# Kernel tuning notes

Measured on AMD Instinct MI355X. Metric: run time of the kernel, lower is better.

The kernel has to match this reference:

```python
import jax, jax.numpy as jnp
import numpy as np

QS, B, C, H, M = 512, 8, 1024, 16, 1536
HC = C // H
KS = QS  # xk = xv = xq (self-attention)


def setup_inputs() -> dict:
    key = jax.random.key(0)
    ks = jax.random.split(key, 16)
    scale = 1.0 / np.sqrt(C)
    xq = jax.random.normal(ks[0], (QS, B, C), jnp.float32)
    memory_kv = jax.random.normal(ks[1], (M, B, H, 2 * HC), jnp.float32)
    memory_length = jax.random.randint(ks[2], (B,), 0, M)
    pad = jax.random.randint(ks[3], (B,), 0, KS)
    mask = jnp.zeros((QS, KS, B), dtype=bool)
    Wq = jax.random.normal(ks[4], (C, C), jnp.float32) * scale
    bq = jax.random.normal(ks[5], (C,), jnp.float32) * 0.02
    Wk = jax.random.normal(ks[6], (C, C), jnp.float32) * scale
    bk = jax.random.normal(ks[7], (C,), jnp.float32) * 0.02
    Wv = jax.random.normal(ks[8], (C, C), jnp.float32) * scale
    bv = jax.random.normal(ks[9], (C,), jnp.float32) * 0.02
    Wo = jax.random.normal(ks[10], (C, C), jnp.float32) * scale
    bo = jax.random.normal(ks[11], (C,), jnp.float32) * 0.02
    return dict(xq=xq, pad=pad, mask=mask, memory_length=memory_length,
                memory_kv=memory_kv, Wq=Wq, bq=bq, Wk=Wk, bk=bk,
                Wv=Wv, bv=bv, Wo=Wo, bo=bo)


def _memory_attention(xq, pad, mask, memory_length, memory_kv,
                      Wq, bq, Wk, bk, Wv, bv, Wo, bo):
    qs, b, c = xq.shape
    m = memory_kv.shape[0]
    T = m + KS  # combined kv length (static upper bound = max(memory_length)+pad)

    # qkv projections (torch Linear: x @ W.T + b), layout (seq, batch, h, hc)
    q = (xq @ Wq.T + bq).reshape(qs, b, H, HC)
    k = (xq @ Wk.T + bk).reshape(KS, b, H, HC)
    v = (xq @ Wv.T + bv).reshape(KS, b, H, HC)

    # cat_padded_seqs as a static-shape gather: slot t of batch i is
    #   memory[t]        if t <  memory_length[i]
    #   new[t - len_i]   if t - len_i < pad[i]
    #   padding (masked) otherwise
    t = jnp.arange(T)[:, None]                      # [T,1]
    L = memory_length[None, :]                      # [1,b]
    in_mem = t < L                                  # [T,b]
    off = t - L                                     # [T,b] offset into new seq
    in_new = (off >= 0) & (off < pad[None, :])      # [T,b]
    idx_new = jnp.clip(off, 0, KS - 1)              # [T,b]

    mem_k = memory_kv[..., :HC]
    mem_v = memory_kv[..., HC:]
    mem_idx = jnp.minimum(jnp.arange(T), m - 1)     # [T]
    k_mem = mem_k[mem_idx]                          # [T,b,H,HC]
    v_mem = mem_v[mem_idx]

    gidx = jnp.broadcast_to(idx_new[:, :, None, None], (T, b, H, HC))
    k_new = jnp.take_along_axis(k, gidx, axis=0)    # [T,b,H,HC]
    v_new = jnp.take_along_axis(v, gidx, axis=0)

    sel = in_mem[:, :, None, None]
    k_comb = jnp.where(sel, k_mem, k_new)
    v_comb = jnp.where(sel, v_mem, v_new)

    # combined padding/user mask, True = masked out
    midx = jnp.broadcast_to(idx_new[None, :, :], (qs, T, b))
    user_m = jnp.take_along_axis(mask, midx, axis=1)        # [qs,T,b]
    comb_mask = jnp.where(in_mem[None], False,
                          jnp.where(in_new[None], user_m, True))

    # attention
    temperature = 1.0 / np.sqrt(HC)
    a = jnp.einsum('sbhc,tbhc->stbh', q, k_comb) * temperature
    a = jnp.where(comb_mask[:, :, :, None], -jnp.inf, a)
    p = jax.nn.softmax(a, axis=1)
    p = jnp.nan_to_num(p)  # fully-masked rows -> 0 (matches torch)
    x = jnp.einsum('stbh,tbhc->sbhc', p, v_comb).reshape(qs, b, c)
    return x @ Wo.T + bo


def reference(xq, pad, mask, memory_length, memory_kv,
              Wq, bq, Wk, bk, Wv, bv, Wo, bo):
    return _memory_attention(xq, pad, mask, memory_length, memory_kv,
                             Wq, bq, Wk, bk, Wv, bv, Wo, bo)
```

## Files before the change

### kernel.cpp

```cpp
#include <hip/hip_runtime.h>

#define QS_ 512
#define B_  8
#define C_  1024
#define H_  16
#define HC_ 64
#define M_  1536
#define KS_ 512
#define TMX 2048

typedef __attribute__((ext_vector_type(8))) short bf16x8;
typedef __attribute__((ext_vector_type(4))) float f32x4;

__device__ __forceinline__ short f2bf(float f) {
    unsigned u = __float_as_uint(f);
    unsigned r = (u + 0x7FFF + ((u >> 16) & 1)) >> 16;
    return (short)r;
}

__device__ __forceinline__ void gload_lds16(const void* g, void* l) {
    __builtin_amdgcn_global_load_lds(
        (const __attribute__((address_space(1))) unsigned int*)g,
        (__attribute__((address_space(3))) unsigned int*)l, 16, 0, 0);
}

__global__ __launch_bounds__(256) void prep_all(
    const float* __restrict__ xq,
    const float* __restrict__ w0, const float* __restrict__ w1,
    const float* __restrict__ w2, const float* __restrict__ w3,
    short* __restrict__ xqb,
    short* __restrict__ d0, short* __restrict__ d1,
    short* __restrict__ d2, short* __restrict__ d3,
    const float* __restrict__ mkv, short* __restrict__ kall,
    short* __restrict__ vall,
    const unsigned char* __restrict__ maskb, const int* __restrict__ mlen,
    const int* __restrict__ padv, unsigned char* __restrict__ mbits)
{
    __shared__ short T[64][72];
    const int bx = blockIdx.x;
    const int tid = threadIdx.x;

    if (bx < 4096) {
        int idx = bx * 256 + tid;
        const float* src; short* dst; int i;
        if (idx < 524288) { src = xq; dst = xqb; i = idx; }
        else {
            int sel = (idx >> 17) & 3;
            i = idx & 131071;
            src = sel == 0 ? w0 : sel == 1 ? w1 : sel == 2 ? w2 : w3;
            dst = sel == 0 ? d0 : sel == 1 ? d1 : sel == 2 ? d2 : d3;
        }
        const float4* s = (const float4*)src + (size_t)i * 2;
        float4 a = s[0], bq = s[1];
        short o[8];
        o[0] = f2bf(a.x);  o[1] = f2bf(a.y);  o[2] = f2bf(a.z);  o[3] = f2bf(a.w);
        o[4] = f2bf(bq.x); o[5] = f2bf(bq.y); o[6] = f2bf(bq.z); o[7] = f2bf(bq.w);
        *(uint4*)(dst + (size_t)i * 8) = *(uint4*)o;
        return;
    }

    if (bx < 7168) {
        const int idx = bx - 4096;
        const int tc = idx % 24;
        const int h  = (idx / 24) & 15;
        const int b  = idx / 384;
        const int L = mlen[b];
        const int tendb = L + padv[b];
        if (tc * 64 >= tendb) return;
        const int row = tid >> 2, part = tid & 3;
        const int t = tc * 64 + row;
        const int g = b * H_ + h;
        const bool skiprow = (t >= L) && (t < L + 512);
        short o[32];
        if (!skiprow) {
            const float4* src = (const float4*)(mkv + (((size_t)t * B_ + b) * H_ + h) * 128 + part * 32);
#pragma unroll
            for (int j = 0; j < 8; ++j) {
                float4 f = src[j];
                o[j * 4 + 0] = f2bf(f.x); o[j * 4 + 1] = f2bf(f.y);
                o[j * 4 + 2] = f2bf(f.z); o[j * 4 + 3] = f2bf(f.w);
            }
        } else {
#pragma unroll
            for (int j = 0; j < 32; ++j) o[j] = 0;
        }
        if (part < 2) {
            if (!skiprow) {
                short* d = kall + ((size_t)g * TMX + t) * 64 + part * 32;
#pragma unroll
                for (int j = 0; j < 4; ++j) ((uint4*)d)[j] = ((uint4*)o)[j];
            }
        } else {
            int hc0 = (part - 2) * 32;
#pragma unroll
            for (int j = 0; j < 32; ++j) T[hc0 + j][row] = o[j];
        }
        __syncthreads();
        const int hc = tid >> 2, seg = tid & 3;
        uint4 a = *(const uint4*)&T[hc][seg * 16];
        uint4 c = *(const uint4*)&T[hc][seg * 16 + 8];
        short* d = vall + ((size_t)g * HC_ + hc) * TMX + tc * 64 + seg * 16;
        ((uint4*)d)[0] = a; ((uint4*)d)[1] = c;
        return;
    }

    if (bx < 7296) {
        const int i = bx - 7168;
        const int b = i >> 4, h = i & 15;
        const int L = mlen[b], P = padv[b];
        const int te = L + P;
        const int z0 = max(1536, L + 512);
        const int z1 = min(2048, (te + 63) & ~63);
        if (z1 > z0) {
            const int g = b * 16 + h;
            const int hc = tid >> 2;
            short* rowp = vall + ((size_t)g * HC_ + hc) * TMX;
            for (int c = z0 + (tid & 3); c < z1; c += 4) rowp[c] = 0;
        }
        return;
    }

    {
        const int j = bx - 7296;
        const int b = j >> 6;
        const int q = (j & 63) * 8 + (tid >> 5);
        const int wordIdx = tid & 31;
        const int L = mlen[b], P = padv[b];
        const int tb = wordIdx * 64;
        unsigned long long w;
        if (tb + 63 < L) {
            w = 0ull;
        } else if (tb >= L + P) {
            w = ~0ull;
        } else {
            w = 0ull;
            const unsigned char* mq = maskb + (size_t)q * (KS_ * B_) + b;
#pragma unroll 4
            for (int k = 0; k < 64; ++k) {
                int t = tb + k;
                int bit;
                if (t < L) bit = 0;
                else {
                    int off = t - L;
                    bit = (off >= P) ? 1 : (mq[(size_t)off * B_] ? 1 : 0);
                }
                w |= (unsigned long long)bit << k;
            }
        }
        ((unsigned long long*)mbits)[(((size_t)(b * 512 + q)) << 5) + wordIdx] = w;
    }
}

template <int EPI>
__device__ __forceinline__ void gemm128_body(
    short (*As)[64], short (*Ws)[64],
    const short* __restrict__ A, const short* __restrict__ W,
    const float* __restrict__ bias, void* __restrict__ outv,
    int n0, int j0, float oscale, const int* __restrict__ mlen)
{
    const int tid  = threadIdx.x;
    const int lane = tid & 63;
    const int wave = tid >> 6;
    const int wm = (wave & 1) * 64;
    const int wn = (wave >> 1) * 64;
    const int lr = lane & 15;
    const int quad = lane >> 4;

    f32x4 acc[4][4];
#pragma unroll
    for (int i = 0; i < 4; ++i)
#pragma unroll
        for (int j = 0; j < 4; ++j)
            acc[i][j] = (f32x4){0.f, 0.f, 0.f, 0.f};

    for (int k0 = 0; k0 < C_; k0 += 64) {
#pragma unroll
        for (int p = 0; p < 4; ++p) {
            int flat = p * 256 + tid;
            int r = flat >> 3, c8 = (flat & 7) * 8;
            gload_lds16(A + (size_t)(n0 + r) * C_ + k0 + c8, (short*)As + flat * 8);
        }
#pragma unroll
        for (int p = 0; p < 4; ++p) {
            int flat = p * 256 + tid;
            int r = flat >> 3, c8 = (flat & 7) * 8;
            gload_lds16(W + (size_t)(j0 + r) * C_ + k0 + c8, (short*)Ws + flat * 8);
        }
        __syncthreads();
#pragma unroll
        for (int ks = 0; ks < 2; ++ks) {
            const int kk = ks * 32 + quad * 8;
            bf16x8 afrag[4], bfrag[4];
#pragma unroll
            for (int im = 0; im < 4; ++im)
                afrag[im] = *(const bf16x8*)&As[wm + im * 16 + lr][kk];
#pragma unroll
            for (int jn = 0; jn < 4; ++jn)
                bfrag[jn] = *(const bf16x8*)&Ws[wn + jn * 16 + lr][kk];
#pragma unroll
            for (int im = 0; im < 4; ++im)
#pragma unroll
                for (int jn = 0; jn < 4; ++jn)
                    acc[im][jn] = __builtin_amdgcn_mfma_f32_16x16x32_bf16(
                        afrag[im], bfrag[jn], acc[im][jn], 0, 0, 0);
        }
        __syncthreads();
    }

    if constexpr (EPI == 2 || EPI == 3) {
        int ml[8];
#pragma unroll
        for (int i = 0; i < 8; ++i) ml[i] = mlen[i];
#pragma unroll
        for (int jn = 0; jn < 4; ++jn) {
            const int col = j0 + wn + jn * 16 + lr;
            const int h = col >> 6, hc = col & 63;
            const float bv = bias[col];
#pragma unroll
            for (int im = 0; im < 4; ++im) {
                const int row = n0 + wm + im * 16 + quad * 4;
#pragma unroll
                for (int r = 0; r < 4; ++r) {
                    const int rr = row + r;
                    const int s = rr >> 3, b = rr & 7;
                    float v = acc[im][jn][r] + bv;
                    if (EPI == 2)
                        ((short*)outv)[((size_t)((b * 16 + h) * TMX) + ml[b] + s) * 64 + hc] = f2bf(v);
                    else
                        ((short*)outv)[((size_t)((b * 16 + h) * 64 + hc)) * TMX + ml[b] + s] = f2bf(v);
                }
            }
        }
    } else {
#pragma unroll
        for (int jn = 0; jn < 4; ++jn) {
            const int col = j0 + wn + jn * 16 + lr;
            const float bv = bias[col];
#pragma unroll
            for (int im = 0; im < 4; ++im) {
                const int row = n0 + wm + im * 16 + quad * 4;
#pragma unroll
                for (int r = 0; r < 4; ++r) {
                    float v = (acc[im][jn][r] + bv) * oscale;
                    if (EPI == 1)
                        ((short*)outv)[(size_t)(row + r) * C_ + col] = f2bf(v);
                    else
                        ((float*)outv)[(size_t)(row + r) * C_ + col] = v;
                }
            }
        }
    }
}

__global__ __launch_bounds__(256) void gemm128_f32(
    const short* __restrict__ A, const short* __restrict__ W,
    const float* __restrict__ bias, float* __restrict__ outv)
{
    __shared__ short As[128][64];
    __shared__ short Ws[128][64];
    gemm128_body<0>(As, Ws, A, W, bias, outv,
                    blockIdx.x * 128, blockIdx.y * 128, 1.0f, nullptr);
}

__global__ __launch_bounds__(256) void gemm128_qkv(
    const short* __restrict__ A,
    const short* __restrict__ Wq, const short* __restrict__ Wk,
    const short* __restrict__ Wv,
    const float* __restrict__ bq, const float* __restrict__ bk,
    const float* __restrict__ bv,
    short* __restrict__ oq, short* __restrict__ kall, short* __restrict__ vall,
    const int* __restrict__ mlen)
{
    __shared__ short As[128][64];
    __shared__ short Ws[128][64];
    const int sel = blockIdx.y >> 3;
    const int n0 = blockIdx.x * 128;
    const int j0 = (blockIdx.y & 7) * 128;
    if (sel == 0)
        gemm128_body<1>(As, Ws, A, Wq, bq, oq, n0, j0, 0.125f, nullptr);
    else if (sel == 1)
        gemm128_body<2>(As, Ws, A, Wk, bk, kall, n0, j0, 1.0f, mlen);
    else
        gemm128_body<3>(As, Ws, A, Wv, bv, vall, n0, j0, 1.0f, mlen);
}

__global__ __launch_bounds__(256, 4) void attn_block(
    const short* __restrict__ qb, const short* __restrict__ kall,
    const short* __restrict__ vall, const unsigned char* __restrict__ mbits,
    const int* __restrict__ mlen, const int* __restrict__ padv,
    short* __restrict__ xout)
{
    __shared__ short Ks[2][64][64];
    __shared__ short Vs[2][64][64];

    const int tid  = threadIdx.x;
    const int lane = tid & 63;
    const int wave = tid >> 6;
    const int lr   = lane & 15;
    const int quad = lane >> 4;
    const int bx = blockIdx.x;
    const int g  = ((bx >> 6) << 3) | (bx & 7);
    const int qg = (bx >> 3) & 7;
    const int b  = g >> 4, h = g & 15;
    const int tend = mlen[b] + padv[b];
    const float NEG = -1e30f;

    const int q = qg * 64 + wave * 16 + lr;

    const short* qrow = qb + ((size_t)q * B_ + b) * C_ + h * HC_;
    bf16x8 q0 = *(const bf16x8*)(qrow + quad * 8);
    bf16x8 q1 = *(const bf16x8*)(qrow + 32 + quad * 8);

    const char* kg = (const char*)(kall + (size_t)g * TMX * 64);
    const char* vg = (const char*)(vall + (size_t)g * HC_ * TMX);
    const unsigned char* mrow = mbits + ((size_t)(b * 512 + q) << 8);

    f32x4 O[4];
#pragma unroll
    for (int i = 0; i < 4; ++i) O[i] = (f32x4){0.f, 0.f, 0.f, 0.f};
    float mr = NEG, lsum = 0.f;

    const int nch = (tend + 63) >> 6;

    auto stage = [&](int t0, int buf) {
        char* KsB = (char*)Ks[buf];
        char* VsB = (char*)Vs[buf];
#pragma unroll
        for (int i = 0; i < 4; ++i) {
            int p = wave * 4 + i;
            int f = ((p & 7) << 6) + lane;
            int row = f >> 3;
            int c = ((f & 7) << 4) ^ ((row & 7) << 4);
            if (p < 8)
                gload_lds16(kg + (size_t)(t0 + row) * 128 + c,
                            KsB + (size_t)f * 16);
            else
                gload_lds16(vg + (size_t)row * (TMX * 2) + (size_t)t0 * 2 + c,
                            VsB + (size_t)f * 16);
        }
    };

    if (nch > 0) stage(0, 0);
    __syncthreads();

    int cur = 0;
    for (int ci = 0; ci < nch; ++ci) {
        const int t0 = ci << 6;

        unsigned long long mw = *(const unsigned long long*)(mrow + (t0 >> 3));

        if (ci + 1 < nch) stage((ci + 1) << 6, cur ^ 1);

        const char* KsB = (const char*)Ks[cur];
        const char* VsB = (const char*)Vs[cur];

        bf16x8 kf[4][2];
#pragma unroll
        for (int tt = 0; tt < 4; ++tt) {
            int t = tt * 16 + lr;
            int sw = (t & 7) << 4;
            kf[tt][0] = *(const bf16x8*)(KsB + t * 128 + ((quad * 16) ^ sw));
            kf[tt][1] = *(const bf16x8*)(KsB + t * 128 + ((64 + quad * 16) ^ sw));
        }

        __builtin_amdgcn_s_setprio(1);
        f32x4 S[4];
#pragma unroll
        for (int tt = 0; tt < 4; ++tt) {
            f32x4 z = (f32x4){0.f, 0.f, 0.f, 0.f};
            z = __builtin_amdgcn_mfma_f32_16x16x32_bf16(kf[tt][0], q0, z, 0, 0, 0);
            S[tt] = __builtin_amdgcn_mfma_f32_16x16x32_bf16(kf[tt][1], q1, z, 0, 0, 0);
        }
        __builtin_amdgcn_s_setprio(0);

        bf16x8 vf[4][2];
#pragma unroll
        for (int ht = 0; ht < 4; ++ht) {
            int hc = ht * 16 + lr;
            int sw = (hc & 7) << 4;
            vf[ht][0] = *(const bf16x8*)(VsB + hc * 128 + ((quad * 16) ^ sw));
            vf[ht][1] = *(const bf16x8*)(VsB + hc * 128 + ((64 + quad * 16) ^ sw));
        }

        float p4[4][4];
#pragma unroll
        for (int tt = 0; tt < 4; ++tt) {
            unsigned m4 = ((unsigned)(mw >> (tt * 16 + quad * 4))) & 15u;
#pragma unroll
            for (int r = 0; r < 4; ++r)
                p4[tt][r] = (m4 & (1u << r)) ? NEG : S[tt][r];
        }

        float rm = NEG;
#pragma unroll
        for (int tt = 0; tt < 4; ++tt)
#pragma unroll
            for (int r = 0; r < 4; ++r) rm = fmaxf(rm, p4[tt][r]);
        rm = fmaxf(rm, __shfl_xor(rm, 16, 64));
        rm = fmaxf(rm, __shfl_xor(rm, 32, 64));
        const float nm = fmaxf(fmaxf(mr, rm), -1e20f);
        const float al = __expf(mr - nm);
        float rs = 0.f;
#pragma unroll
        for (int tt = 0; tt < 4; ++tt)
#pragma unroll
            for (int r = 0; r < 4; ++r) {
                float e = __expf(p4[tt][r] - nm);
                p4[tt][r] = e;
                rs += e;
            }
        rs += __shfl_xor(rs, 16, 64);
        rs += __shfl_xor(rs, 32, 64);
        lsum = lsum * al + rs;
        mr = nm;
#pragma unroll
        for (int ht = 0; ht < 4; ++ht)
#pragma unroll
            for (int r = 0; r < 4; ++r) O[ht][r] *= al;

        bf16x8 pf[2];
        const int slA = ((quad & 1) * 2) * 16 + lr;
        const int slB = slA + 16;
        const unsigned sel = (quad & 2) ? 0x07060302u : 0x05040100u;
#pragma unroll
        for (int hf = 0; hf < 2; ++hf) {
            const int tt0 = hf * 2;
            unsigned pk[4];
#pragma unroll
            for (int r = 0; r < 4; ++r) {
                unsigned o;
                asm("v_cvt_pk_bf16_f32 %0, %1, %2"
                    : "=v"(o) : "v"(p4[tt0][r]), "v"(p4[tt0 + 1][r]));
                pk[r] = o;
            }
            unsigned uA[4], uB[4];
#pragma unroll
            for (int r = 0; r < 4; ++r) {
                uA[r] = (unsigned)__shfl((int)pk[r], slA, 64);
                uB[r] = (unsigned)__shfl((int)pk[r], slB, 64);
            }
            unsigned wv[4];
            wv[0] = __builtin_amdgcn_perm(uA[1], uA[0], sel);
            wv[1] = __builtin_amdgcn_perm(uA[3], uA[2], sel);
            wv[2] = __builtin_amdgcn_perm(uB[1], uB[0], sel);
            wv[3] = __builtin_amdgcn_perm(uB[3], uB[2], sel);
            pf[hf] = *(const bf16x8*)wv;
        }

        __builtin_amdgcn_s_setprio(1);
#pragma unroll
        for (int ht = 0; ht < 4; ++ht) {
            O[ht] = __builtin_amdgcn_mfma_f32_16x16x32_bf16(vf[ht][0], pf[0], O[ht], 0, 0, 0);
            O[ht] = __builtin_amdgcn_mfma_f32_16x16x32_bf16(vf[ht][1], pf[1], O[ht], 0, 0, 0);
        }
        __builtin_amdgcn_s_setprio(0);

        __syncthreads();
        cur ^= 1;
    }

    float inv = (lsum > 0.f) ? 1.0f / lsum : 0.f;
#pragma unroll
    for (int ht = 0; ht < 4; ++ht) {
        short ov[4];
#pragma unroll
        for (int r = 0; r < 4; ++r) ov[r] = f2bf(O[ht][r] * inv);
        short* d = xout + ((size_t)q * B_ + b) * C_ + h * HC_ + ht * 16 + quad * 4;
        *(long long*)d = *(const long long*)ov;
    }
}

extern "C" void kernel_launch(void* const* d_in, const int* in_sizes, int n_in,
                              void* d_out, int out_size, void* d_ws, size_t ws_size,
                              hipStream_t stream)
{
    const float* xq   = (const float*)d_in[0];
    const int*   pad  = (const int*)d_in[1];
    const unsigned char* maskb = (const unsigned char*)d_in[2];
    const int*   mlen = (const int*)d_in[3];
    const float* mkv  = (const float*)d_in[4];
    const float* Wq   = (const float*)d_in[5];
    const float* bq   = (const float*)d_in[6];
    const float* Wk   = (const float*)d_in[7];
    const float* bk   = (const float*)d_in[8];
    const float* Wv   = (const float*)d_in[9];
    const float* bv   = (const float*)d_in[10];
    const float* Wo   = (const float*)d_in[11];
    const float* bo   = (const float*)d_in[12];
    float* out = (float*)d_out;

    short* xqb  = (short*)d_ws;
    short* wqb  = xqb  + (size_t)4194304;
    short* wkb  = wqb  + (size_t)1048576;
    short* wvb  = wkb  + (size_t)1048576;
    short* wob  = wvb  + (size_t)1048576;
    short* kall = wob  + (size_t)1048576;
    short* vall = kall + (size_t)128 * TMX * 64;
    short* qbuf = vall + (size_t)128 * HC_ * TMX;
    short* xbuf = qbuf + (size_t)4194304;
    unsigned char* mbits = (unsigned char*)(xbuf + (size_t)4194304);

    dim3 gblk(256);
    prep_all<<<dim3(7808), gblk, 0, stream>>>(
        xq, Wq, Wk, Wv, Wo, xqb, wqb, wkb, wvb, wob,
        mkv, kall, vall, maskb, mlen, pad, mbits);

    gemm128_qkv<<<dim3(32, 24), gblk, 0, stream>>>(
        xqb, wqb, wkb, wvb, bq, bk, bv, qbuf, kall, vall, mlen);

    attn_block<<<dim3(1024), gblk, 0, stream>>>(qbuf, kall, vall, mbits,
                                                mlen, pad, xbuf);

    gemm128_f32<<<dim3(32, 8), gblk, 0, stream>>>(xbuf, wob, bo, out);
}
```

Measured before the change: 332.9 us.

## Fuse memory-KV staging and mask bits into QKV GEMM launch; swizzle GEMM LDS

Splits the conversion prep into its own kernel and moves the memory-KV bf16 staging, V-tail zeroing and mask-bit building into the same launch as the QKV projection GEMM. The intent is for the bandwidth-bound memory copy to overlap with the compute-bound GEMM blocks. The V transpose store now skips columns the GEMM writes, avoiding a write race. It also XOR-swizzles the GEMM's LDS tiles to cut bank conflicts and sets occupancy hints of 3 on the GEMM kernels.

After: 303.6 us. 8.8% less time.

```diff
diff --git a/kernel.cpp b/kernel.cpp
--- a/kernel.cpp
+++ b/kernel.cpp
@@ -24,43 +24,171 @@
         (__attribute__((address_space(3))) unsigned int*)l, 16, 0, 0);
 }
 
-__global__ __launch_bounds__(256) void prep_all(
+__global__ __launch_bounds__(256) void prep_cvt(
     const float* __restrict__ xq,
     const float* __restrict__ w0, const float* __restrict__ w1,
     const float* __restrict__ w2, const float* __restrict__ w3,
     short* __restrict__ xqb,
     short* __restrict__ d0, short* __restrict__ d1,
-    short* __restrict__ d2, short* __restrict__ d3,
-    const float* __restrict__ mkv, short* __restrict__ kall,
-    short* __restrict__ vall,
+    short* __restrict__ d2, short* __restrict__ d3)
+{
+    int idx = blockIdx.x * 256 + threadIdx.x;
+    const float* src; short* dst; int i;
+    if (idx < 524288) { src = xq; dst = xqb; i = idx; }
+    else {
+        int sel = (idx >> 17) & 3;
+        i = idx & 131071;
+        src = sel == 0 ? w0 : sel == 1 ? w1 : sel == 2 ? w2 : w3;
+        dst = sel == 0 ? d0 : sel == 1 ? d1 : sel == 2 ? d2 : d3;
+    }
+    const float4* s = (const float4*)src + (size_t)i * 2;
+    float4 a = s[0], bq = s[1];
+    short o[8];
+    o[0] = f2bf(a.x);  o[1] = f2bf(a.y);  o[2] = f2bf(a.z);  o[3] = f2bf(a.w);
+    o[4] = f2bf(bq.x); o[5] = f2bf(bq.y); o[6] = f2bf(bq.z); o[7] = f2bf(bq.w);
+    *(uint4*)(dst + (size_t)i * 8) = *(uint4*)o;
+}
+
+template <int EPI>
+__device__ __forceinline__ void gemm128_body(
+    short (*As)[64], short (*Ws)[64],
+    const short* __restrict__ A, const short* __restrict__ W,
+    const float* __restrict__ bias, void* __restrict__ outv,
+    int n0, int j0, float oscale, const int* __restrict__ mlen)
+{
+    const int tid  = threadIdx.x;
+    const int lane = tid & 63;
+    const int wave = tid >> 6;
+    const int wm = (wave & 1) * 64;
+    const int wn = (wave >> 1) * 64;
+    const int lr = lane & 15;
+    const int quad = lane >> 4;
+
+    f32x4 acc[4][4];
+#pragma unroll
+    for (int i = 0; i < 4; ++i)
+#pragma unroll
+        for (int j = 0; j < 4; ++j)
+            acc[i][j] = (f32x4){0.f, 0.f, 0.f, 0.f};
+
+    for (int k0 = 0; k0 < C_; k0 += 64) {
+#pragma unroll
+        for (int p = 0; p < 4; ++p) {
+            int flat = p * 256 + tid;
+            int r = flat >> 3;
+            int c8 = ((flat & 7) ^ (r & 7)) * 8;
+            gload_lds16(A + (size_t)(n0 + r) * C_ + k0 + c8, (short*)As + flat * 8);
+        }
+#pragma unroll
+        for (int p = 0; p < 4; ++p) {
+            int flat = p * 256 + tid;
+            int r = flat >> 3;
+            int c8 = ((flat & 7) ^ (r & 7)) * 8;
+            gload_lds16(W + (size_t)(j0 + r) * C_ + k0 + c8, (short*)Ws + flat * 8);
+        }
+        __syncthreads();
+#pragma unroll
+        for (int ks = 0; ks < 2; ++ks) {
+            const int kkb = (ks * 32 + quad * 8) * 2;
+            bf16x8 afrag[4], bfrag[4];
+#pragma unroll
+            for (int im = 0; im < 4; ++im) {
+                int row = wm + im * 16 + lr;
+                afrag[im] = *(const bf16x8*)((const char*)As + row * 128 + (kkb ^ ((row & 7) << 4)));
+            }
+#pragma unroll
+            for (int jn = 0; jn < 4; ++jn) {
+                int row = wn + jn * 16 + lr;
+                bfrag[jn] = *(const bf16x8*)((const char*)Ws + row * 128 + (kkb ^ ((row & 7) << 4)));
+            }
+#pragma unroll
+            for (int im = 0; im < 4; ++im)
+#pragma unroll
+                for (int jn = 0; jn < 4; ++jn)
+                    acc[im][jn] = __builtin_amdgcn_mfma_f32_16x16x32_bf16(
+                        afrag[im], bfrag[jn], acc[im][jn], 0, 0, 0);
+        }
+        __syncthreads();
+    }
+
+    if constexpr (EPI == 2 || EPI == 3) {
+        int ml[8];
+#pragma unroll
+        for (int i = 0; i < 8; ++i) ml[i] = mlen[i];
+#pragma unroll
+        for (int jn = 0; jn < 4; ++jn) {
+            const int col = j0 + wn + jn * 16 + lr;
+            const int h = col >> 6, hc = col & 63;
+            const float bv = bias[col];
+#pragma unroll
+            for (int im = 0; im < 4; ++im) {
+                const int row = n0 + wm + im * 16 + quad * 4;
+#pragma unroll
+                for (int r = 0; r < 4; ++r) {
+                    const int rr = row + r;
+                    const int s = rr >> 3, b = rr & 7;
+                    float v = acc[im][jn][r] + bv;
+                    if (EPI == 2)
+                        ((short*)outv)[((size_t)((b * 16 + h) * TMX) + ml[b] + s) * 64 + hc] = f2bf(v);
+                    else
+                        ((short*)outv)[((size_t)((b * 16 + h) * 64 + hc)) * TMX + ml[b] + s] = f2bf(v);
+                }
+            }
+        }
+    } else {
+#pragma unroll
+        for (int jn = 0; jn < 4; ++jn) {
+            const int col = j0 + wn + jn * 16 + lr;
+            const float bv = bias[col];
+#pragma unroll
+            for (int im = 0; im < 4; ++im) {
+                const int row = n0 + wm + im * 16 + quad * 4;
+#pragma unroll
+                for (int r = 0; r < 4; ++r) {
+                    float v = (acc[im][jn][r] + bv) * oscale;
+                    if (EPI == 1)
+                        ((short*)outv)[(size_t)(row + r) * C_ + col] = f2bf(v);
+                    else
+                        ((float*)outv)[(size_t)(row + r) * C_ + col] = v;
+                }
+            }
+        }
+    }
+}
+
+__global__ __launch_bounds__(256, 3) void qkv_plus(
+    const short* __restrict__ Axq,
+    const short* __restrict__ Wq, const short* __restrict__ Wk,
+    const short* __restrict__ Wv,
+    const float* __restrict__ bq, const float* __restrict__ bk,
+    const float* __restrict__ bv,
+    short* __restrict__ oq, short* __restrict__ kall, short* __restrict__ vall,
+    const float* __restrict__ mkv,
     const unsigned char* __restrict__ maskb, const int* __restrict__ mlen,
     const int* __restrict__ padv, unsigned char* __restrict__ mbits)
 {
-    __shared__ short T[64][72];
+    __shared__ short As[128][64];
+    __shared__ short Ws[128][64];
     const int bx = blockIdx.x;
     const int tid = threadIdx.x;
 
-    if (bx < 4096) {
-        int idx = bx * 256 + tid;
-        const float* src; short* dst; int i;
-        if (idx < 524288) { src = xq; dst = xqb; i = idx; }
-        else {
-            int sel = (idx >> 17) & 3;
-            i = idx & 131071;
-            src = sel == 0 ? w0 : sel == 1 ? w1 : sel == 2 ? w2 : w3;
-            dst = sel == 0 ? d0 : sel == 1 ? d1 : sel == 2 ? d2 : d3;
-        }
-        const float4* s = (const float4*)src + (size_t)i * 2;
-        float4 a = s[0], bq = s[1];
-        short o[8];
-        o[0] = f2bf(a.x);  o[1] = f2bf(a.y);  o[2] = f2bf(a.z);  o[3] = f2bf(a.w);
-        o[4] = f2bf(bq.x); o[5] = f2bf(bq.y); o[6] = f2bf(bq.z); o[7] = f2bf(bq.w);
-        *(uint4*)(dst + (size_t)i * 8) = *(uint4*)o;
+    if (bx < 768) {
+        const int sel = bx >> 8;
+        const int t = bx & 255;
+        const int n0 = (t >> 3) * 128;
+        const int j0 = (t & 7) * 128;
+        if (sel == 0)
+            gemm128_body<1>(As, Ws, Axq, Wq, bq, oq, n0, j0, 0.125f, nullptr);
+        else if (sel == 1)
+            gemm128_body<2>(As, Ws, Axq, Wk, bk, kall, n0, j0, 1.0f, mlen);
+        else
+            gemm128_body<3>(As, Ws, Axq, Wv, bv, vall, n0, j0, 1.0f, mlen);
         return;
     }
 
-    if (bx < 7168) {
-        const int idx = bx - 4096;
+    if (bx < 3840) {
+        short (*T)[72] = (short(*)[72])&As[0][0];
+        const int idx = bx - 768;
         const int tc = idx % 24;
         const int h  = (idx / 24) & 15;
         const int b  = idx / 384;
@@ -97,15 +225,24 @@
         }
         __syncthreads();
         const int hc = tid >> 2, seg = tid & 3;
-        uint4 a = *(const uint4*)&T[hc][seg * 16];
-        uint4 c = *(const uint4*)&T[hc][seg * 16 + 8];
-        short* d = vall + ((size_t)g * HC_ + hc) * TMX + tc * 64 + seg * 16;
-        ((uint4*)d)[0] = a; ((uint4*)d)[1] = c;
+        const int c0 = tc * 64 + seg * 16;
+        short* d = vall + ((size_t)g * HC_ + hc) * TMX + c0;
+        const short* srow = &T[hc][seg * 16];
+        if (c0 + 16 <= L || c0 >= L + 512) {
+            ((uint4*)d)[0] = *(const uint4*)&srow[0];
+            ((uint4*)d)[1] = *(const uint4*)&srow[8];
+        } else if (!(c0 >= L && c0 + 16 <= L + 512)) {
+#pragma unroll
+            for (int j = 0; j < 16; ++j) {
+                int tt = c0 + j;
+                if (tt < L || tt >= L + 512) d[j] = srow[j];
+            }
+        }
         return;
     }
 
-    if (bx < 7296) {
-        const int i = bx - 7168;
+    if (bx < 3968) {
+        const int i = bx - 3840;
         const int b = i >> 4, h = i & 15;
         const int L = mlen[b], P = padv[b];
         const int te = L + P;
@@ -121,7 +258,7 @@
     }
 
     {
-        const int j = bx - 7296;
+        const int j = bx - 3968;
         const int b = j >> 6;
         const int q = (j & 63) * 8 + (tid >> 5);
         const int wordIdx = tid & 31;
@@ -151,108 +288,7 @@
     }
 }
 
-template <int EPI>
-__device__ __forceinline__ void gemm128_body(
-    short (*As)[64], short (*Ws)[64],
-    const short* __restrict__ A, const short* __restrict__ W,
-    const float* __restrict__ bias, void* __restrict__ outv,
-    int n0, int j0, float oscale, const int* __restrict__ mlen)
-{
-    const int tid  = threadIdx.x;
-    const int lane = tid & 63;
-    const int wave = tid >> 6;
-    const int wm = (wave & 1) * 64;
-    const int wn = (wave >> 1) * 64;
-    const int lr = lane & 15;
-    const int quad = lane >> 4;
-
-    f32x4 acc[4][4];
-#pragma unroll
-    for (int i = 0; i < 4; ++i)
-#pragma unroll
-        for (int j = 0; j < 4; ++j)
-            acc[i][j] = (f32x4){0.f, 0.f, 0.f, 0.f};
-
-    for (int k0 = 0; k0 < C_; k0 += 64) {
-#pragma unroll
-        for (int p = 0; p < 4; ++p) {
-            int flat = p * 256 + tid;
-            int r = flat >> 3, c8 = (flat & 7) * 8;
-            gload_lds16(A + (size_t)(n0 + r) * C_ + k0 + c8, (short*)As + flat * 8);
-        }
-#pragma unroll
-        for (int p = 0; p < 4; ++p) {
-            int flat = p * 256 + tid;
-            int r = flat >> 3, c8 = (flat & 7) * 8;
-            gload_lds16(W + (size_t)(j0 + r) * C_ + k0 + c8, (short*)Ws + flat * 8);
-        }
-        __syncthreads();
-#pragma unroll
-        for (int ks = 0; ks < 2; ++ks) {
-            const int kk = ks * 32 + quad * 8;
-            bf16x8 afrag[4], bfrag[4];
-#pragma unroll
-            for (int im = 0; im < 4; ++im)
-                afrag[im] = *(const bf16x8*)&As[wm + im * 16 + lr][kk];
-#pragma unroll
-            for (int jn = 0; jn < 4; ++jn)
-                bfrag[jn] = *(const bf16x8*)&Ws[wn + jn * 16 + lr][kk];
-#pragma unroll
-            for (int im = 0; im < 4; ++im)
-#pragma unroll
-                for (int jn = 0; jn < 4; ++jn)
-                    acc[im][jn] = __builtin_amdgcn_mfma_f32_16x16x32_bf16(
-                        afrag[im], bfrag[jn], acc[im][jn], 0, 0, 0);
-        }
-        __syncthreads();
-    }
-
-    if constexpr (EPI == 2 || EPI == 3) {
-        int ml[8];
-#pragma unroll
-        for (int i = 0; i < 8; ++i) ml[i] = mlen[i];
-#pragma unroll
-        for (int jn = 0; jn < 4; ++jn) {
-            const int col = j0 + wn + jn * 16 + lr;
-            const int h = col >> 6, hc = col & 63;
-            const float bv = bias[col];
-#pragma unroll
-            for (int im = 0; im < 4; ++im) {
-                const int row = n0 + wm + im * 16 + quad * 4;
-#pragma unroll
-                for (int r = 0; r < 4; ++r) {
-                    const int rr = row + r;
-                    const int s = rr >> 3, b = rr & 7;
-                    float v = acc[im][jn][r] + bv;
-                    if (EPI == 2)
-                        ((short*)outv)[((size_t)((b * 16 + h) * TMX) + ml[b] + s) * 64 + hc] = f2bf(v);
-                    else
-                        ((short*)outv)[((size_t)((b * 16 + h) * 64 + hc)) * TMX + ml[b] + s] = f2bf(v);
-                }
-            }
-        }
-    } else {
-#pragma unroll
-        for (int jn = 0; jn < 4; ++jn) {
-            const int col = j0 + wn + jn * 16 + lr;
-            const float bv = bias[col];
-#pragma unroll
-            for (int im = 0; im < 4; ++im) {
-                const int row = n0 + wm + im * 16 + quad * 4;
-#pragma unroll
-                for (int r = 0; r < 4; ++r) {
-                    float v = (acc[im][jn][r] + bv) * oscale;
-                    if (EPI == 1)
-                        ((short*)outv)[(size_t)(row + r) * C_ + col] = f2bf(v);
-                    else
-                        ((float*)outv)[(size_t)(row + r) * C_ + col] = v;
-                }
-            }
-        }
-    }
-}
-
-__global__ __launch_bounds__(256) void gemm128_f32(
+__global__ __launch_bounds__(256, 3) void gemm128_f32(
     const short* __restrict__ A, const short* __restrict__ W,
     const float* __restrict__ bias, float* __restrict__ outv)
 {
@@ -260,28 +296,6 @@
     __shared__ short Ws[128][64];
     gemm128_body<0>(As, Ws, A, W, bias, outv,
                     blockIdx.x * 128, blockIdx.y * 128, 1.0f, nullptr);
-}
-
-__global__ __launch_bounds__(256) void gemm128_qkv(
-    const short* __restrict__ A,
-    const short* __restrict__ Wq, const short* __restrict__ Wk,
-    const short* __restrict__ Wv,
-    const float* __restrict__ bq, const float* __restrict__ bk,
-    const float* __restrict__ bv,
-    short* __restrict__ oq, short* __restrict__ kall, short* __restrict__ vall,
-    const int* __restrict__ mlen)
-{
-    __shared__ short As[128][64];
-    __shared__ short Ws[128][64];
-    const int sel = blockIdx.y >> 3;
-    const int n0 = blockIdx.x * 128;
-    const int j0 = (blockIdx.y & 7) * 128;
-    if (sel == 0)
-        gemm128_body<1>(As, Ws, A, Wq, bq, oq, n0, j0, 0.125f, nullptr);
-    else if (sel == 1)
-        gemm128_body<2>(As, Ws, A, Wk, bk, kall, n0, j0, 1.0f, mlen);
-    else
-        gemm128_body<3>(As, Ws, A, Wv, bv, vall, n0, j0, 1.0f, mlen);
 }
 
 __global__ __launch_bounds__(256, 4) void attn_block(
@@ -501,12 +515,12 @@
     unsigned char* mbits = (unsigned char*)(xbuf + (size_t)4194304);
 
     dim3 gblk(256);
-    prep_all<<<dim3(7808), gblk, 0, stream>>>(
-        xq, Wq, Wk, Wv, Wo, xqb, wqb, wkb, wvb, wob,
-        mkv, kall, vall, maskb, mlen, pad, mbits);
-
-    gemm128_qkv<<<dim3(32, 24), gblk, 0, stream>>>(
-        xqb, wqb, wkb, wvb, bq, bk, bv, qbuf, kall, vall, mlen);
+    prep_cvt<<<dim3(4096), gblk, 0, stream>>>(
+        xq, Wq, Wk, Wv, Wo, xqb, wqb, wkb, wvb, wob);
+
+    qkv_plus<<<dim3(4480), gblk, 0, stream>>>(
+        xqb, wqb, wkb, wvb, bq, bk, bv, qbuf, kall, vall,
+        mkv, maskb, mlen, pad, mbits);
 
     attn_block<<<dim3(1024), gblk, 0, stream>>>(qbuf, kall, vall, mbits,
                                                 mlen, pad, xbuf);
```
